# Performance work log

Measured on AMD Instinct MI355X. Metric: run time of the kernel, lower is better.

## Reference

```python
import jax, jax.numpy as jnp
import numpy as np

B, C, H, W, KS = 8, 3, 512, 512, 3
K = KS * KS  # kernel_elements = 9


def setup_inputs() -> dict:
    key = jax.random.key(0)
    ks = jax.random.split(key, 5)
    return {
        "x": jax.random.normal(ks[0], (B, C, H, W), jnp.float32),
        "w1": jax.random.normal(ks[1], (K - 1, C, KS, KS), jnp.float32) * 0.1,  # find_ref conv weight
        "b1": jax.random.normal(ks[2], (K - 1,), jnp.float32) * 0.1,
        "w2": jax.random.normal(ks[3], (C, K), jnp.float32) * 0.1,  # grouped 1x1 conv: C groups, K in-ch each
        "b2": jax.random.normal(ks[4], (C,), jnp.float32) * 0.1,
    }


def _grid_sample_bilinear(img_nhwc, gx, gy):
    # torch.grid_sample, mode='bilinear', padding_mode='zeros', align_corners=False
    # img_nhwc: [B,H,W,C]; gx,gy: [B,h,w,K] normalized coords (x=width, y=height)
    Bs, Hh, Ww, _ = img_nhwc.shape
    ix = ((gx + 1.0) * Ww - 1.0) * 0.5
    iy = ((gy + 1.0) * Hh - 1.0) * 0.5
    ix0 = jnp.floor(ix)
    iy0 = jnp.floor(iy)
    wx1 = ix - ix0
    wy1 = iy - iy0
    wx0 = 1.0 - wx1
    wy0 = 1.0 - wy1
    bidx = jnp.arange(Bs)[:, None, None, None]

    def corner(yc, xc, wgt):
        valid = (xc >= 0) & (xc < Ww) & (yc >= 0) & (yc < Hh)
        xi = jnp.clip(xc, 0, Ww - 1).astype(jnp.int32)
        yi = jnp.clip(yc, 0, Hh - 1).astype(jnp.int32)
        v = img_nhwc[bidx, yi, xi]  # [B,h,w,K,C]
        return v * (wgt * valid)[..., None]

    out = corner(iy0, ix0, wy0 * wx0)
    out = out + corner(iy0, ix0 + 1.0, wy0 * wx1)
    out = out + corner(iy0 + 1.0, ix0, wy1 * wx0)
    out = out + corner(iy0 + 1.0, ix0 + 1.0, wy1 * wx1)
    return out  # [B,h,w,K,C]


def _forward(x, w1, b1, w2, b2):
    Bs, Cc, Hh, Ww = x.shape
    pad = KS // 2
    # find_ref: conv3x3 (pad=1) + sigmoid -> offsets in [0,1]
    off = jax.lax.conv_general_dilated(
        x, w1, (1, 1), ((pad, pad), (pad, pad)),
        dimension_numbers=("NCHW", "OIHW", "NCHW"))
    off = jax.nn.sigmoid(off + b1[None, :, None, None])  # [B,K-1,H,W]
    off = jnp.transpose(off, (0, 2, 3, 1)).reshape(Bs, Hh, Ww, (K - 1) // 2, 2)
    ctr = float(KS // 2)
    sym = 2.0 * ctr - off  # find_symmetric_points
    center = jnp.zeros((Bs, Hh, Ww, 1, 2), off.dtype)
    off_all = jnp.concatenate([off, center, sym], axis=-2)  # [B,H,W,K,2]
    # base grid: stack(h_grid, w_grid) with linspace(0,1)
    base = jnp.stack(
        jnp.meshgrid(jnp.linspace(0.0, 1.0, Hh), jnp.linspace(0.0, 1.0, Ww), indexing="ij"),
        axis=-1)  # [H,W,2]
    coords = base[None, :, :, None, :] + off_all  # [B,H,W,K,2]
    # grid_sample interprets last dim as (x=width, y=height)
    gx = coords[..., 0]
    gy = coords[..., 1]
    img = jnp.transpose(x, (0, 2, 3, 1))  # [B,H,W,C]
    sampled = _grid_sample_bilinear(img, gx, gy)  # [B,H,W,K,C]
    # concatenation order in torch: elem-major channels -> [B, K*C, H, W]
    deformed = jnp.transpose(sampled, (0, 3, 4, 1, 2)).reshape(Bs, K * Cc, Hh, Ww)
    # grouped 1x1 conv: groups=C, group g consumes channels [g*K:(g+1)*K]
    grp = deformed.reshape(Bs, Cc, K, Hh, Ww)
    out = jnp.einsum("bgkhw,gk->bghw", grp, w2) + b2[None, :, None, None]
    return jax.nn.relu(out)


def reference(x, w1, b1, w2, b2):
    return _forward(x, w1, b1, w2, b2)
```

## Files before the change

kernel.cpp:

```cpp
#include <hip/hip_runtime.h>

#define BATCH 8
#define HDIM  512
#define WDIM  512
#define PLANE (HDIM * WDIM)

#define QN      129
#define QPAIRS  (QN * QN)
#define QPLANE  (4 * QPAIRS * 8)
#define IMG12   (5 * QPLANE)
#define PACKBYTES ((size_t)BATCH * IMG12)
#define W1E_FLOATS (27 * 8)

#define QC_N      129
#define YROW0     254
#define YROWS     259
#define YSTRIDE   260
#define QSTRIDE   (YSTRIDE * 16)
#define PARSTRIDE (QC_N * QSTRIDE)
#define IMGSTRIDE (2 * PARSTRIDE)

typedef _Float16 half2v __attribute__((ext_vector_type(2)));
typedef _Float16 half4v __attribute__((ext_vector_type(4)));
typedef _Float16 half8v __attribute__((ext_vector_type(8)));
typedef float    f2v    __attribute__((ext_vector_type(2)));

struct __align__(16) HQuad { half2v p0, p1, p2, p3; };
struct __align__(8)  HPair { half2v lo, hi; };

#if __has_builtin(__builtin_amdgcn_fdot2)
#define FDOT2(a, b, c) __builtin_amdgcn_fdot2((a), (b), (c), false)
#else
#define FDOT2(a, b, c) fmaf((float)(a).x, (float)(b).x, fmaf((float)(a).y, (float)(b).y, (c)))
#endif

#if __has_builtin(__builtin_amdgcn_exp2f)
#define EXP2F(x) __builtin_amdgcn_exp2f(x)
#else
#define EXP2F(x) exp2f(x)
#endif

__global__ __launch_bounds__(256) void repack_dots(
    const float* __restrict__ x,
    const float* __restrict__ w1,
    const float* __restrict__ w2,
    char* __restrict__ xp)
{
    if (blockIdx.x == 0 && threadIdx.x < W1E_FLOATS) {
        int t = threadIdx.x;
        float* w1e = (float*)(xp + PACKBYTES);
        w1e[t] = w1[(t & 7) * 27 + (t >> 3)];
    }

    int b  = blockIdx.x & 7;
    int P  = (blockIdx.x >> 3) & 3;
    int Qy = blockIdx.x >> 5;
    int Qx = threadIdx.x;
    if (Qx >= QN) return;
    int px = P & 1, py = P >> 1;
    int X0 = 2 * Qx + 254 + px;
    int Y0 = 2 * Qy + 254 + py;

    const float* xb = x + (size_t)b * 3 * PLANE;

    float vc[4][3];
#pragma unroll
    for (int cy = 0; cy < 2; cy++)
#pragma unroll
        for (int cx = 0; cx < 2; cx++) {
            int xx = X0 + cx, yy = Y0 + cy;
            bool vld = (xx <= 511) && (yy <= 511);
            int xs = min(xx, 511), ys = min(yy, 511);
            int base = (ys << 9) + xs;
            int ci = cy * 2 + cx;
            vc[ci][0] = vld ? xb[base]             : 0.f;
            vc[ci][1] = vld ? xb[PLANE + base]     : 0.f;
            vc[ci][2] = vld ? xb[2 * PLANE + base] : 0.f;
        }

    char* dst = xp + (size_t)b * IMG12 + (size_t)((P * QPAIRS + Qy * QN + Qx) << 3);
#pragma unroll
    for (int q = 0; q < 5; q++) {
        float wa = w2[3 * q], wb = w2[3 * q + 1], wc = w2[3 * q + 2];
        half4v o;
#pragma unroll
        for (int ci = 0; ci < 4; ci++) {
            float v = fmaf(vc[ci][2], wc, fmaf(vc[ci][1], wb, vc[ci][0] * wa));
            o[ci] = (_Float16)v;
        }
        *(half4v*)(dst + q * QPLANE) = o;
    }
}

__global__ __launch_bounds__(256) void seesaw_v13(
    const float* __restrict__ x,
    const char* __restrict__ xpack,
    const float* __restrict__ b1,
    const float* __restrict__ w2, const float* __restrict__ b2,
    float* __restrict__ out)
{
    int t    = threadIdx.x;
    int b    = blockIdx.x & 7;
    int rest = blockIdx.x >> 3;
    int i    = rest >> 1;
    int j    = ((rest & 1) << 8) + t;

    const float* xb = x + (size_t)b * 3 * PLANE;
    const char*  hb = xpack + (size_t)b * IMG12;
    const f2v*   wv = (const f2v*)(xpack + PACKBYTES);

    float tap[27];
    int cm1 = j - 1; if (cm1 < 0) cm1 = 0;
    int cp1 = j + 1; if (cp1 > 511) cp1 = 511;
    bool jlo = (j == 0), jhi = (j == 511);

    if (i >= 1 && i <= 510) {
#pragma unroll
        for (int di = 0; di < 3; di++) {
            const float* row = xb + ((i + di - 1) << 9);
#pragma unroll
            for (int c = 0; c < 3; c++) {
                const float* rc = row + c * PLANE;
                float vm = rc[cm1]; if (jlo) vm = 0.f;
                float v0 = rc[j];
                float vp = rc[cp1]; if (jhi) vp = 0.f;
                tap[c * 9 + di * 3 + 0] = vm;
                tap[c * 9 + di * 3 + 1] = v0;
                tap[c * 9 + di * 3 + 2] = vp;
            }
        }
    } else {
#pragma unroll
        for (int di = 0; di < 3; di++) {
            int y = i + di - 1;
            bool yv = (unsigned)y < (unsigned)HDIM;
            const float* row = xb + ((yv ? y : 0) << 9);
#pragma unroll
            for (int c = 0; c < 3; c++) {
                const float* rc = row + c * PLANE;
                float vm = rc[cm1]; if (jlo || !yv) vm = 0.f;
                float v0 = rc[j];   if (!yv)        v0 = 0.f;
                float vp = rc[cp1]; if (jhi || !yv) vp = 0.f;
                tap[c * 9 + di * 3 + 0] = vm;
                tap[c * 9 + di * 3 + 1] = v0;
                tap[c * 9 + di * 3 + 2] = vp;
            }
        }
    }
    __builtin_amdgcn_sched_barrier(0);

    f2v acc2[4];
#pragma unroll
    for (int eh = 0; eh < 4; eh++) { acc2[eh][0] = b1[2 * eh]; acc2[eh][1] = b1[2 * eh + 1]; }
#pragma unroll
    for (int k = 0; k < 27; k++) {
        f2v tk; tk[0] = tap[k]; tk[1] = tap[k];
#pragma unroll
        for (int eh = 0; eh < 4; eh++)
            acc2[eh] = __builtin_elementwise_fma(tk, wv[k * 4 + eh], acc2[eh]);
    }

    const float NLOG2E = -1.44269504f;
    float s256[8];
#pragma unroll
    for (int e = 0; e < 8; e++) {
        float acc = acc2[e >> 1][e & 1];
        s256[e] = 256.0f * __builtin_amdgcn_rcpf(1.0f + EXP2F(acc * NLOG2E));
    }

    const float k511 = 256.0f / 511.0f;
    float fxb = fmaf((float)i, k511, 255.5f);
    float fyb = fmaf((float)j, k511, 255.5f);

    int   adr[5];
    float wX[5][2], wY[5][2];
#pragma unroll
    for (int q = 0; q < 5; q++) {
        float ixf = (q < 4) ? (fxb + s256[2 * q])     : fxb;
        float iyf = (q < 4) ? (fyb + s256[2 * q + 1]) : fyb;
        int ix0 = (int)ixf, iy0 = (int)iyf;
        float wx1 = ixf - (float)ix0, wy1 = iyf - (float)iy0;
        wX[q][0] = (ix0 <= 511) ? (1.f - wx1) : 0.f;
        wX[q][1] = (ix0 <= 510) ? wx1 : 0.f;
        wY[q][0] = (iy0 <= 511) ? (1.f - wy1) : 0.f;
        wY[q][1] = (iy0 <= 510) ? wy1 : 0.f;
        int x0c = min(ix0, 511), y0c = min(iy0, 511);
        int P  = ((y0c & 1) << 1) | (x0c & 1);
        int Qx = (x0c >> 1) - 127;
        int Qy = (y0c >> 1) - 127;
        adr[q] = (P * QPAIRS + Qy * QN + Qx) << 3;
    }

    HPair pv[5];
#pragma unroll
    for (int q = 0; q < 5; q++)
        pv[q] = *(const HPair*)(hb + (size_t)(q * QPLANE + adr[q]));
    __builtin_amdgcn_sched_barrier(0);

    float og[3] = {0.f, 0.f, 0.f};
#pragma unroll
    for (int q = 0; q < 5; q++) {
        int g = q / 3;
        float v00 = (float)pv[q].lo[0], v01 = (float)pv[q].lo[1];
        float v10 = (float)pv[q].hi[0], v11c = (float)pv[q].hi[1];
        float r0 = fmaf(v01,  wX[q][1], v00 * wX[q][0]);
        float r1 = fmaf(v11c, wX[q][1], v10 * wX[q][0]);
        og[g] = fmaf(r1, wY[q][1], fmaf(r0, wY[q][0], og[g]));
    }

    if ((i | j) == 0) {
#pragma unroll
        for (int p = 5; p < 9; p++) {
            float ixf = fxb + 512.0f - s256[2 * (p - 5)];
            float iyf = fyb + 512.0f - s256[2 * (p - 5) + 1];
            float ix0f = floorf(ixf), iy0f = floorf(iyf);
            float wx1 = ixf - ix0f, wy1 = iyf - iy0f;
            float wx0 = 1.f - wx1,  wy0 = 1.f - wy1;
            int ix0 = (int)ix0f, iy0 = (int)iy0f;
            float t0 = 0.f, t1 = 0.f, t2 = 0.f;
            for (int cy = 0; cy < 2; cy++) {
                int yc2 = iy0 + cy;
                if (yc2 < 0 || yc2 >= HDIM) continue;
                float wy = cy ? wy1 : wy0;
                for (int cx = 0; cx < 2; cx++) {
                    int xcc2 = ix0 + cx;
                    if (xcc2 < 0 || xcc2 >= WDIM) continue;
                    float wgt = wy * (cx ? wx1 : wx0);
                    int base = (yc2 << 9) + xcc2;
                    t0 = fmaf(xb[base],             wgt, t0);
                    t1 = fmaf(xb[PLANE + base],     wgt, t1);
                    t2 = fmaf(xb[2 * PLANE + base], wgt, t2);
                }
            }
            int g  = p / 3;
            int k0 = (p % 3) * 3;
            og[g] = fmaf(t0, w2[g * 9 + k0 + 0], og[g]);
            og[g] = fmaf(t1, w2[g * 9 + k0 + 1], og[g]);
            og[g] = fmaf(t2, w2[g * 9 + k0 + 2], og[g]);
        }
    }

    size_t ob = (size_t)(b * 3) * PLANE + ((size_t)i << 9) + j;
#pragma unroll
    for (int g = 0; g < 3; g++) {
        float vv = og[g] + b2[g];
        out[ob + (size_t)g * PLANE] = vv > 0.f ? vv : 0.f;
    }
}

__global__ __launch_bounds__(256) void repack_tiles(
    const float* __restrict__ x, char* __restrict__ xp)
{
    int b    = blockIdx.x & 7;
    int rest = blockIdx.x >> 3;
    int p    = rest & 1;
    int Qc   = rest >> 1;
    int xb0  = 254 + 2 * Qc + p;
    int x1   = xb0 + 1;
    bool x1v = (x1 < 512);

    const float* xb = x + (size_t)b * 3 * PLANE;
    char* dst = xp + (size_t)b * IMGSTRIDE + (size_t)p * PARSTRIDE
                   + (size_t)Qc * QSTRIDE;

    for (int t = threadIdx.x; t < YROWS; t += 256) {
        int y = YROW0 + t;
        half8v o;
        if (y < 512) {
            int base = (y << 9) + xb0;
            float a0 = xb[base];
            float a1 = xb[PLANE + base];
            float a2 = xb[2 * PLANE + base];
            float b0 = 0.f, b1c = 0.f, b2c = 0.f;
            if (x1v) {
                b0  = xb[base + 1];
                b1c = xb[PLANE + base + 1];
                b2c = xb[2 * PLANE + base + 1];
            }
            o[0] = (_Float16)a0; o[1] = (_Float16)a1; o[2] = (_Float16)a2; o[3] = (_Float16)0.f;
            o[4] = (_Float16)b0; o[5] = (_Float16)b1c; o[6] = (_Float16)b2c; o[7] = (_Float16)0.f;
        } else {
#pragma unroll
            for (int k = 0; k < 8; k++) o[k] = (_Float16)0.f;
        }
        *(half8v*)(dst + (size_t)t * 16) = o;
    }
}

__global__ __launch_bounds__(256) void seesaw_v11(
    const float* __restrict__ x, const char* __restrict__ xpack,
    const float* __restrict__ w1, const float* __restrict__ b1,
    const float* __restrict__ w2, const float* __restrict__ b2,
    float* __restrict__ out)
{
    int t  = threadIdx.x;
    int b  = blockIdx.x & 7;
    int i  = blockIdx.x >> 3;
    int j0 = t << 1;

    const float* xb = x + (size_t)b * 3 * PLANE;
    const char*  hb = xpack + (size_t)b * IMGSTRIDE;

    int cm = j0 - 1; if (cm < 0) cm = 0;
    int cp = j0 + 2; if (cp > 511) cp = 511;
    bool jlo = (t == 0), jhi = (t == 255);

    float vm[9], va[9], vb9[9], vp9[9];
    if (i >= 1 && i <= 510) {
#pragma unroll
        for (int di = 0; di < 3; di++) {
            const float* row = xb + ((i + di - 1) << 9);
#pragma unroll
            for (int c = 0; c < 3; c++) {
                const float* rc = row + c * PLANE;
                float m = rc[cm]; if (jlo) m = 0.f;
                f2v  mid = *(const f2v*)(rc + j0);
                float pv = rc[cp]; if (jhi) pv = 0.f;
                int r = c * 3 + di;
                vm[r] = m; va[r] = mid[0]; vb9[r] = mid[1]; vp9[r] = pv;
            }
        }
    } else {
#pragma unroll
        for (int di = 0; di < 3; di++) {
            int y = i + di - 1;
            bool yv = (unsigned)y < (unsigned)HDIM;
            const float* row = xb + ((yv ? y : 0) << 9);
#pragma unroll
            for (int c = 0; c < 3; c++) {
                const float* rc = row + c * PLANE;
                float m = rc[cm]; if (jlo || !yv) m = 0.f;
                f2v  mid = *(const f2v*)(rc + j0);
                float pv = rc[cp]; if (jhi || !yv) pv = 0.f;
                float m0 = yv ? mid[0] : 0.f;
                float m1 = yv ? mid[1] : 0.f;
                int r = c * 3 + di;
                vm[r] = m; va[r] = m0; vb9[r] = m1; vp9[r] = pv;
            }
        }
    }
    __builtin_amdgcn_sched_barrier(0);

    float tap0[27], tap1[27];
#pragma unroll
    for (int c = 0; c < 3; c++)
#pragma unroll
        for (int di = 0; di < 3; di++) {
            int r = c * 3 + di, k = c * 9 + di * 3;
            tap0[k]     = vm[r];  tap0[k + 1] = va[r];  tap0[k + 2] = vb9[r];
            tap1[k]     = va[r];  tap1[k + 1] = vb9[r]; tap1[k + 2] = vp9[r];
        }

    const float NLOG2E = -1.44269504f;
    auto conv8 = [&](const float* tap, float* s2) {
        f2v V[13];
#pragma unroll
        for (int k = 0; k < 13; k++) { V[k][0] = tap[2 * k]; V[k][1] = tap[2 * k + 1]; }
#pragma unroll
        for (int e = 0; e < 8; e++) {
            const float* we = w1 + e * 27;
            f2v a2; a2[0] = b1[e]; a2[1] = 0.f;
#pragma unroll
            for (int k = 0; k < 13; k++) {
                f2v ww; ww[0] = we[2 * k]; ww[1] = we[2 * k + 1];
                a2 = __builtin_elementwise_fma(V[k], ww, a2);
            }
            float acc = a2[0] + a2[1] + tap[26] * we[26];
            s2[e] = 256.0f * __builtin_amdgcn_rcpf(1.0f + EXP2F(acc * NLOG2E));
        }
    };
    float s0[8], s1[8];
    conv8(tap0, s0);
    conv8(tap1, s1);

    half2v w2a[5], w2b[5];
#pragma unroll
    for (int q = 0; q < 5; q++) {
        w2a[q][0] = (_Float16)w2[q * 3];
        w2a[q][1] = (_Float16)w2[q * 3 + 1];
        w2b[q][0] = (_Float16)w2[q * 3 + 2];
        w2b[q][1] = (_Float16)0.f;
    }

    const float k511 = 256.0f / 511.0f;
    float fxb = fmaf((float)i, k511, 255.5f);
    float fy0 = fmaf((float)j0, k511, 255.5f);
    float fy1 = fy0 + k511;

    int   adrA[5], adrB[5];
    float wXA[5][2], wYA[5][2], wXB[5][2], wYB[5][2];
    auto phase1 = [&](const float* s2, float fyb, int (&adr)[5],
                      float (&wX)[5][2], float (&wY)[5][2]) {
#pragma unroll
        for (int q = 0; q < 5; q++) {
            float ixf = (q < 4) ? (fxb + s2[2 * q])     : fxb;
            float iyf = (q < 4) ? (fyb + s2[2 * q + 1]) : fyb;
            int ix0 = (int)ixf, iy0 = (int)iyf;
            float wx1 = ixf - (float)ix0, wy1 = iyf - (float)iy0;
            wX[q][0] = (ix0 <= 511) ? (1.f - wx1) : 0.f;
            wX[q][1] = (ix0 <= 510) ? wx1 : 0.f;
            wY[q][0] = (iy0 <= 511) ? (1.f - wy1) : 0.f;
            wY[q][1] = (iy0 <= 510) ? wy1 : 0.f;
            int x0c = min(ix0, 511);
            int y0c = min(iy0, 511);
            int Qc  = (x0c >> 1) - 127;
            int off = (Qc << 12) + (Qc << 6) + ((y0c - 254) << 4);
            adr[q] = off + ((x0c & 1) ? PARSTRIDE : 0);
        }
    };

    phase1(s0, fy0, adrA, wXA, wYA);
    HQuad qA[5][2];
#pragma unroll
    for (int q = 0; q < 5; q++) {
        qA[q][0] = *(const HQuad*)(hb + (size_t)adrA[q]);
        qA[q][1] = *(const HQuad*)(hb + (size_t)adrA[q] + 16);
    }
    phase1(s1, fy1, adrB, wXB, wYB);
    HQuad qB[5][2];
#pragma unroll
    for (int q = 0; q < 5; q++) {
        qB[q][0] = *(const HQuad*)(hb + (size_t)adrB[q]);
        qB[q][1] = *(const HQuad*)(hb + (size_t)adrB[q] + 16);
    }
    __builtin_amdgcn_sched_barrier(0);

    float ogA[3] = {0.f, 0.f, 0.f}, ogB[3] = {0.f, 0.f, 0.f};
    auto phase3 = [&](HQuad (&qv)[5][2], float (&wX)[5][2], float (&wY)[5][2], float* og) {
#pragma unroll
        for (int q = 0; q < 5; q++) {
            int g = q / 3;
            float dl0 = FDOT2(qv[q][0].p0, w2a[q], FDOT2(qv[q][0].p1, w2b[q], 0.f));
            float dh0 = FDOT2(qv[q][0].p2, w2a[q], FDOT2(qv[q][0].p3, w2b[q], 0.f));
            float dl1 = FDOT2(qv[q][1].p0, w2a[q], FDOT2(qv[q][1].p1, w2b[q], 0.f));
            float dh1 = FDOT2(qv[q][1].p2, w2a[q], FDOT2(qv[q][1].p3, w2b[q], 0.f));
            float r0 = fmaf(dh0, wX[q][1], dl0 * wX[q][0]);
            float r1 = fmaf(dh1, wX[q][1], dl1 * wX[q][0]);
            og[g] = fmaf(r1, wY[q][1], fmaf(r0, wY[q][0], og[g]));
        }
    };
    phase3(qA, wXA, wYA, ogA);
    phase3(qB, wXB, wYB, ogB);

    if ((i | j0) == 0) {
#pragma unroll
        for (int p = 5; p < 9; p++) {
            float ixf = fxb + 512.0f - s0[2 * (p - 5)];
            float iyf = fy0 + 512.0f - s0[2 * (p - 5) + 1];
            float ix0f = floorf(ixf), iy0f = floorf(iyf);
            float wx1 = ixf - ix0f, wy1 = iyf - iy0f;
            float wx0 = 1.f - wx1,  wy0 = 1.f - wy1;
            int ix0 = (int)ix0f, iy0 = (int)iy0f;
            float t0 = 0.f, t1 = 0.f, t2 = 0.f;
            for (int cy = 0; cy < 2; cy++) {
                int yc2 = iy0 + cy;
                if (yc2 < 0 || yc2 >= HDIM) continue;
                float wy = cy ? wy1 : wy0;
                for (int cx = 0; cx < 2; cx++) {
                    int xcc2 = ix0 + cx;
                    if (xcc2 < 0 || xcc2 >= WDIM) continue;
                    float wgt = wy * (cx ? wx1 : wx0);
                    int base = (yc2 << 9) + xcc2;
                    t0 = fmaf(xb[base],             wgt, t0);
                    t1 = fmaf(xb[PLANE + base],     wgt, t1);
                    t2 = fmaf(xb[2 * PLANE + base], wgt, t2);
                }
            }
            int g  = p / 3;
            int k0 = (p % 3) * 3;
            ogA[g] = fmaf(t0, w2[g * 9 + k0 + 0], ogA[g]);
            ogA[g] = fmaf(t1, w2[g * 9 + k0 + 1], ogA[g]);
            ogA[g] = fmaf(t2, w2[g * 9 + k0 + 2], ogA[g]);
        }
    }

    size_t ob = (size_t)(b * 3) * PLANE + ((size_t)i << 9) + j0;
#pragma unroll
    for (int g = 0; g < 3; g++) {
        float u0 = ogA[g] + b2[g];
        float u1 = ogB[g] + b2[g];
        f2v st;
        st[0] = u0 > 0.f ? u0 : 0.f;
        st[1] = u1 > 0.f ? u1 : 0.f;
        *(f2v*)(out + ob + (size_t)g * PLANE) = st;
    }
}

__global__ __launch_bounds__(256) void seesaw_fused_v1(
    const float* __restrict__ x, const float* __restrict__ w1,
    const float* __restrict__ b1, const float* __restrict__ w2,
    const float* __restrict__ b2, float* __restrict__ out)
{
    int t = threadIdx.x;
    int gid = blockIdx.x * 256 + t;
    int j = gid & (WDIM - 1);
    int i = (gid >> 9) & (HDIM - 1);
    int b = gid >> 18;
    const float* xb = x + (size_t)b * 3 * PLANE;
    float acc[8];
#pragma unroll
    for (int e = 0; e < 8; e++) acc[e] = b1[e];
#pragma unroll
    for (int di = 0; di < 3; di++) {
        int y = i + di - 1;
        if (y < 0 || y >= HDIM) continue;
#pragma unroll
        for (int dj = 0; dj < 3; dj++) {
            int xc = j + dj - 1;
            if (xc < 0 || xc >= WDIM) continue;
            size_t base = (size_t)y * WDIM + xc;
#pragma unroll
            for (int c = 0; c < 3; c++) {
                float v = xb[(size_t)c * PLANE + base];
#pragma unroll
                for (int e = 0; e < 8; e++)
                    acc[e] = fmaf(v, w1[e * 27 + c * 9 + di * 3 + dj], acc[e]);
            }
        }
    }
    float s[8];
#pragma unroll
    for (int e = 0; e < 8; e++) s[e] = 1.0f / (1.0f + __expf(-acc[e]));
    const float inv511 = 1.0f / 511.0f;
    float bx = (float)i * inv511, by = (float)j * inv511;
    float og0 = 0.f, og1 = 0.f, og2 = 0.f;
#pragma unroll
    for (int p = 0; p < 9; p++) {
        float c0, c1;
        if (p < 4)       { c0 = s[2 * p];              c1 = s[2 * p + 1]; }
        else if (p == 4) { c0 = 0.f;                   c1 = 0.f; }
        else             { c0 = 2.0f - s[2 * (p - 5)]; c1 = 2.0f - s[2 * (p - 5) + 1]; }
        float ixf = (bx + c0) * 256.0f + 255.5f;
        float iyf = (by + c1) * 256.0f + 255.5f;
        float ix0f = floorf(ixf), iy0f = floorf(iyf);
        float wx1 = ixf - ix0f, wy1 = iyf - iy0f;
        float wx0 = 1.f - wx1,  wy0 = 1.f - wy1;
        int ix0 = (int)ix0f, iy0 = (int)iy0f;
        float s0 = 0.f, s1 = 0.f, s2 = 0.f;
#pragma unroll
        for (int cy = 0; cy < 2; cy++) {
            int yc = iy0 + cy;
            if (yc < 0 || yc >= HDIM) continue;
            float wy = cy ? wy1 : wy0;
#pragma unroll
            for (int cx = 0; cx < 2; cx++) {
                int xcc = ix0 + cx;
                if (xcc < 0 || xcc >= WDIM) continue;
                float wgt = wy * (cx ? wx1 : wx0);
                size_t base = (size_t)yc * WDIM + xcc;
                s0 = fmaf(xb[base],             wgt, s0);
                s1 = fmaf(xb[PLANE + base],     wgt, s1);
                s2 = fmaf(xb[2 * PLANE + base], wgt, s2);
            }
        }
        int g  = p / 3;
        int k0 = (p % 3) * 3;
        float* og = (g == 0) ? &og0 : (g == 1) ? &og1 : &og2;
        *og = fmaf(s0, w2[g * 9 + k0 + 0], *og);
        *og = fmaf(s1, w2[g * 9 + k0 + 1], *og);
        *og = fmaf(s2, w2[g * 9 + k0 + 2], *og);
    }
    size_t ob = (size_t)(b * 3) * PLANE + (size_t)i * WDIM + j;
    float v0 = og0 + b2[0], v1 = og1 + b2[1], v2 = og2 + b2[2];
    out[ob]             = v0 > 0.f ? v0 : 0.f;
    out[ob + PLANE]     = v1 > 0.f ? v1 : 0.f;
    out[ob + 2 * PLANE] = v2 > 0.f ? v2 : 0.f;
}

extern "C" void kernel_launch(void* const* d_in, const int* in_sizes, int n_in,
                              void* d_out, int out_size, void* d_ws, size_t ws_size,
                              hipStream_t stream) {
    const float* x  = (const float*)d_in[0];
    const float* w1 = (const float*)d_in[1];
    const float* b1 = (const float*)d_in[2];
    const float* w2 = (const float*)d_in[3];
    const float* b2 = (const float*)d_in[4];
    float* out = (float*)d_out;

    int total = BATCH * HDIM * WDIM;
    size_t need13 = PACKBYTES + W1E_FLOATS * 4 + 64;
    size_t need11 = (size_t)BATCH * IMGSTRIDE + 16;

    if (ws_size >= need13) {
        repack_dots<<<8 * 4 * QN, 256, 0, stream>>>(x, w1, w2, (char*)d_ws);
        seesaw_v13<<<total / 256, 256, 0, stream>>>(x, (const char*)d_ws,
                                                    b1, w2, b2, out);
    } else if (ws_size >= need11) {
        repack_tiles<<<8 * 2 * QC_N, 256, 0, stream>>>(x, (char*)d_ws);
        seesaw_v11<<<BATCH * HDIM, 256, 0, stream>>>(x, (const char*)d_ws,
                                                     w1, b1, w2, b2, out);
    } else {
        seesaw_fused_v1<<<total / 256, 256, 0, stream>>>(x, w1, b1, w2, b2, out);
    }
}
```

Measured before the change: 121.1 us.

## Repack sampled image into y-contiguous column strips to improve gather locality

```diff
diff --git a/kernel.cpp b/kernel.cpp
--- a/kernel.cpp
+++ b/kernel.cpp
@@ -5,11 +5,10 @@
 #define WDIM  512
 #define PLANE (HDIM * WDIM)
 
-#define QN      129
-#define QPAIRS  (QN * QN)
-#define QPLANE  (4 * QPAIRS * 8)
-#define IMG12   (5 * QPLANE)
-#define PACKBYTES ((size_t)BATCH * IMG12)
+#define COLB   1040
+#define NCOL   1290
+#define IMG15  ((size_t)NCOL * COLB)
+#define PACK15 ((size_t)BATCH * IMG15)
 #define W1E_FLOATS (27 * 8)
 
 #define QC_N      129
@@ -21,12 +20,11 @@
 #define IMGSTRIDE (2 * PARSTRIDE)
 
 typedef _Float16 half2v __attribute__((ext_vector_type(2)));
-typedef _Float16 half4v __attribute__((ext_vector_type(4)));
 typedef _Float16 half8v __attribute__((ext_vector_type(8)));
 typedef float    f2v    __attribute__((ext_vector_type(2)));
 
 struct __align__(16) HQuad { half2v p0, p1, p2, p3; };
-struct __align__(8)  HPair { half2v lo, hi; };
+struct __align__(4)  HPair4 { half2v lo, hi; };
 
 #if __has_builtin(__builtin_amdgcn_fdot2)
 #define FDOT2(a, b, c) __builtin_amdgcn_fdot2((a), (b), (c), false)
@@ -40,7 +38,7 @@
 #define EXP2F(x) exp2f(x)
 #endif
 
-__global__ __launch_bounds__(256) void repack_dots(
+__global__ __launch_bounds__(256) void repack_cols(
     const float* __restrict__ x,
     const float* __restrict__ w1,
     const float* __restrict__ w2,
@@ -48,51 +46,47 @@
 {
     if (blockIdx.x == 0 && threadIdx.x < W1E_FLOATS) {
         int t = threadIdx.x;
-        float* w1e = (float*)(xp + PACKBYTES);
+        float* w1e = (float*)(xp + PACK15);
         w1e[t] = w1[(t & 7) * 27 + (t >> 3)];
     }
 
     int b  = blockIdx.x & 7;
-    int P  = (blockIdx.x >> 3) & 3;
-    int Qy = blockIdx.x >> 5;
-    int Qx = threadIdx.x;
-    if (Qx >= QN) return;
-    int px = P & 1, py = P >> 1;
-    int X0 = 2 * Qx + 254 + px;
-    int Y0 = 2 * Qy + 254 + py;
-
+    int by = blockIdx.x >> 3;
+    int y  = 254 + by;
     const float* xb = x + (size_t)b * 3 * PLANE;
-
-    float vc[4][3];
-#pragma unroll
-    for (int cy = 0; cy < 2; cy++)
-#pragma unroll
-        for (int cx = 0; cx < 2; cx++) {
-            int xx = X0 + cx, yy = Y0 + cy;
-            bool vld = (xx <= 511) && (yy <= 511);
-            int xs = min(xx, 511), ys = min(yy, 511);
-            int base = (ys << 9) + xs;
-            int ci = cy * 2 + cx;
-            vc[ci][0] = vld ? xb[base]             : 0.f;
-            vc[ci][1] = vld ? xb[PLANE + base]     : 0.f;
-            vc[ci][2] = vld ? xb[2 * PLANE + base] : 0.f;
-        }
-
-    char* dst = xp + (size_t)b * IMG12 + (size_t)((P * QPAIRS + Qy * QN + Qx) << 3);
-#pragma unroll
-    for (int q = 0; q < 5; q++) {
-        float wa = w2[3 * q], wb = w2[3 * q + 1], wc = w2[3 * q + 2];
-        half4v o;
-#pragma unroll
-        for (int ci = 0; ci < 4; ci++) {
-            float v = fmaf(vc[ci][2], wc, fmaf(vc[ci][1], wb, vc[ci][0] * wa));
-            o[ci] = (_Float16)v;
-        }
-        *(half4v*)(dst + q * QPLANE) = o;
+    char* dst = xp + (size_t)b * IMG15;
+
+    for (int t = threadIdx.x; t < 258; t += 256) {
+        int x0 = 254 + t;
+        int px = t & 1;
+        int Qx = (x0 >> 1) - 127;
+        float a0 = 0.f, a1 = 0.f, a2 = 0.f;
+        float c0 = 0.f, c1 = 0.f, c2 = 0.f;
+        if (y < 512) {
+            const float* row = xb + (y << 9);
+            a0 = row[x0];
+            a1 = row[PLANE + x0];
+            a2 = row[2 * PLANE + x0];
+            if (x0 < 511) {
+                c0 = row[x0 + 1];
+                c1 = row[PLANE + x0 + 1];
+                c2 = row[2 * PLANE + x0 + 1];
+            }
+        }
+        char* colbase = dst + (size_t)by * 4;
+#pragma unroll
+        for (int q = 0; q < 5; q++) {
+            float wa = w2[3 * q], wb = w2[3 * q + 1], wc = w2[3 * q + 2];
+            half2v e;
+            e[0] = (_Float16)fmaf(a2, wc, fmaf(a1, wb, a0 * wa));
+            e[1] = (_Float16)fmaf(c2, wc, fmaf(c1, wb, c0 * wa));
+            int col = ((q << 1) + px) * 129 + Qx;
+            *(half2v*)(colbase + (size_t)col * COLB) = e;
+        }
     }
 }
 
-__global__ __launch_bounds__(256) void seesaw_v13(
+__global__ __launch_bounds__(256) void seesaw_v15(
     const float* __restrict__ x,
     const char* __restrict__ xpack,
     const float* __restrict__ b1,
@@ -106,8 +100,8 @@
     int j    = ((rest & 1) << 8) + t;
 
     const float* xb = x + (size_t)b * 3 * PLANE;
-    const char*  hb = xpack + (size_t)b * IMG12;
-    const f2v*   wv = (const f2v*)(xpack + PACKBYTES);
+    const char*  hb = xpack + (size_t)b * IMG15;
+    const f2v*   wv = (const f2v*)(xpack + PACK15);
 
     float tap[27];
     int cm1 = j - 1; if (cm1 < 0) cm1 = 0;
@@ -147,7 +141,6 @@
             }
         }
     }
-    __builtin_amdgcn_sched_barrier(0);
 
     f2v acc2[4];
 #pragma unroll
@@ -185,16 +178,15 @@
         wY[q][0] = (iy0 <= 511) ? (1.f - wy1) : 0.f;
         wY[q][1] = (iy0 <= 510) ? wy1 : 0.f;
         int x0c = min(ix0, 511), y0c = min(iy0, 511);
-        int P  = ((y0c & 1) << 1) | (x0c & 1);
-        int Qx = (x0c >> 1) - 127;
-        int Qy = (y0c >> 1) - 127;
-        adr[q] = (P * QPAIRS + Qy * QN + Qx) << 3;
-    }
-
-    HPair pv[5];
+        int pxq = x0c & 1;
+        int Qx  = (x0c >> 1) - 127;
+        adr[q] = (((q << 1) + pxq) * 129 + Qx) * COLB + ((y0c - 254) << 2);
+    }
+
+    HPair4 pv[5];
 #pragma unroll
     for (int q = 0; q < 5; q++)
-        pv[q] = *(const HPair*)(hb + (size_t)(q * QPLANE + adr[q]));
+        pv[q] = *(const HPair4*)(hb + (size_t)adr[q]);
     __builtin_amdgcn_sched_barrier(0);
 
     float og[3] = {0.f, 0.f, 0.f};
@@ -578,12 +570,12 @@
     float* out = (float*)d_out;
 
     int total = BATCH * HDIM * WDIM;
-    size_t need13 = PACKBYTES + W1E_FLOATS * 4 + 64;
+    size_t need15 = PACK15 + W1E_FLOATS * 4 + 64;
     size_t need11 = (size_t)BATCH * IMGSTRIDE + 16;
 
-    if (ws_size >= need13) {
-        repack_dots<<<8 * 4 * QN, 256, 0, stream>>>(x, w1, w2, (char*)d_ws);
-        seesaw_v13<<<total / 256, 256, 0, stream>>>(x, (const char*)d_ws,
+    if (ws_size >= need15) {
+        repack_cols<<<8 * 259, 256, 0, stream>>>(x, w1, w2, (char*)d_ws);
+        seesaw_v15<<<total / 256, 256, 0, stream>>>(x, (const char*)d_ws,
                                                     b1, w2, b2, out);
     } else if (ws_size >= need11) {
         repack_tiles<<<8 * 2 * QC_N, 256, 0, stream>>>(x, (char*)d_ws);
```

Measured after the change: 122.2 us. No clear change (+0.9%).
